# Kernel optimization log

Hardware: AMD Instinct MI355X
Metric: run time of the kernel (lower is better)

Reference implementation:

```python
import jax, jax.numpy as jnp
import numpy as np
import math

L, B, S, D, H, F, C = 2, 2, 1024, 512, 32, 2048, 1000
EPS_LN = 1e-5

def _grid_coords(batch, seq_len):
    g = math.ceil(math.sqrt(seq_len))
    xs = jnp.linspace(0.0, 1.0, g)
    gx, gy = jnp.meshgrid(xs, xs, indexing='ij')
    pts = jnp.stack([gx.ravel(), gy.ravel()], axis=1)
    reps = math.ceil(seq_len / (g * g))
    pts = jnp.tile(pts, (reps, 1))[:seq_len]
    return jnp.broadcast_to(pts[None], (batch, seq_len, 2)).astype(jnp.float32)

def setup_inputs() -> dict:
    key = jax.random.key(0)
    ks = iter(jax.random.split(key, 16))
    sd = 0.02
    inp = {
        'x': jax.random.normal(next(ks), (B, S, D), jnp.float32),
        'coords': _grid_coords(B, S),
        'Wq': jax.random.normal(next(ks), (L, D, D), jnp.float32) * sd,
        'Wk': jax.random.normal(next(ks), (L, D, D), jnp.float32) * sd,
        'Wv': jax.random.normal(next(ks), (L, D, D), jnp.float32) * sd,
        'rot_w1': jax.random.normal(next(ks), (L, 3, H), jnp.float32) * 0.5,
        'rot_b1': jnp.zeros((L, H), jnp.float32),
        'rot_w2': jax.random.normal(next(ks), (L, H), jnp.float32) * 0.1,
        'rot_b2': jnp.zeros((L,), jnp.float32),
        'trans_w1': jax.random.normal(next(ks), (L, 2, H), jnp.float32) * 0.5,
        'trans_b1': jnp.zeros((L, H), jnp.float32),
        'trans_w2': jax.random.normal(next(ks), (L, H), jnp.float32) * 0.1,
        'trans_b2': jnp.zeros((L,), jnp.float32),
        'refl_w1': jax.random.normal(next(ks), (L, 4, H), jnp.float32) * 0.5,
        'refl_b1': jnp.zeros((L, H), jnp.float32),
        'refl_w2': jax.random.normal(next(ks), (L, H), jnp.float32) * 0.1,
        'refl_b2': jnp.zeros((L,), jnp.float32),
        'ln1_g': jnp.ones((L, D), jnp.float32),
        'ln1_b': jnp.zeros((L, D), jnp.float32),
        'ffn_w1': jax.random.normal(next(ks), (L, D, F), jnp.float32) * sd,
        'ffn_b1': jnp.zeros((L, F), jnp.float32),
        'ffn_w2': jax.random.normal(next(ks), (L, F, D), jnp.float32) * sd,
        'ffn_b2': jnp.zeros((L, D), jnp.float32),
        'ln2_g': jnp.ones((L, D), jnp.float32),
        'ln2_b': jnp.zeros((L, D), jnp.float32),
        'lnf_g': jnp.ones((D,), jnp.float32),
        'lnf_b': jnp.zeros((D,), jnp.float32),
        'fc_w': jax.random.normal(next(ks), (D, C), jnp.float32) * sd,
        'fc_b': jnp.zeros((C,), jnp.float32),
    }
    return inp

def _layernorm(x, g, b):
    mu = x.mean(-1, keepdims=True)
    var = ((x - mu) ** 2).mean(-1, keepdims=True)
    return (x - mu) * jax.lax.rsqrt(var + EPS_LN) * g + b

def _pair_mlp(inp, w1, b1, w2, b2):
    # inp: [B,S,S,f] -> [B,S,S]
    h = jax.nn.relu(jnp.einsum('bijf,fh->bijh', inp, w1) + b1)
    return jnp.einsum('bijh,h->bij', h, w2) + b2

def reference(x, coords, Wq, Wk, Wv, rot_w1, rot_b1, rot_w2, rot_b2,
              trans_w1, trans_b1, trans_w2, trans_b2,
              refl_w1, refl_b1, refl_w2, refl_b2,
              ln1_g, ln1_b, ffn_w1, ffn_b1, ffn_w2, ffn_b2, ln2_g, ln2_b,
              lnf_g, lnf_b, fc_w, fc_b):
    d_model = x.shape[-1]
    scale = math.sqrt(d_model)
    # Pairwise relative geometry (layer-independent): rel = coords_j - coords_i
    rel = coords[:, None, :, :] - coords[:, :, None, :]   # [B,S,S,2]
    dx, dy = rel[..., 0], rel[..., 1]
    dist = jnp.sqrt(dx * dx + dy * dy + 1e-8)
    theta = jnp.arctan2(dy, dx)
    rot_in = jnp.stack([dist, jnp.sin(theta), jnp.cos(theta)], axis=-1)  # [B,S,S,3]
    trans_in = rel                                                       # [B,S,S,2]
    refl_in = jnp.concatenate([rel, -rel], axis=-1)                      # [B,S,S,4]

    n_layers = Wq.shape[0]
    for l in range(n_layers):
        Q = x @ Wq[l]
        K = x @ Wk[l]
        V = x @ Wv[l]
        scores = jnp.einsum('bid,bjd->bij', Q, K) / scale
        scores = scores \
            + _pair_mlp(rot_in, rot_w1[l], rot_b1[l], rot_w2[l], rot_b2[l]) \
            + _pair_mlp(trans_in, trans_w1[l], trans_b1[l], trans_w2[l], trans_b2[l]) \
            + _pair_mlp(refl_in, refl_w1[l], refl_b1[l], refl_w2[l], refl_b2[l])
        attn = jax.nn.softmax(scores, axis=-1)
        attn_out = jnp.einsum('bij,bjd->bid', attn, V)
        x = _layernorm(x + attn_out, ln1_g[l], ln1_b[l])
        ffn = jax.nn.relu(x @ ffn_w1[l] + ffn_b1[l]) @ ffn_w2[l] + ffn_b2[l]
        x = _layernorm(x + ffn, ln2_g[l], ln2_b[l])

    x = _layernorm(x, lnf_g, lnf_b)
    pooled = x.mean(axis=1)          # [B,D]
    return pooled @ fc_w + fc_b      # [B,C]
```

## Files before the change

kernel.cpp:

```cpp
#include <hip/hip_runtime.h>
#include <hip/hip_bf16.h>

using bf16 = __hip_bfloat16;
typedef __attribute__((ext_vector_type(8))) short short8;
typedef __attribute__((ext_vector_type(4))) float f32x4;

constexpr int NLAYER = 2;
constexpr int NB = 2;
constexpr int NS = 1024;
constexpr int ND = 512;
constexpr int NH = 32;
constexpr int NF = 2048;
constexpr int NC = 1000;
constexpr float EPS_LN = 1e-5f;

__device__ inline unsigned short f2bfu(float x) {
    union { bf16 h; unsigned short u; } c;
    c.h = __float2bfloat16(x);
    return c.u;
}

#define GLOAD16(gp, lp) __builtin_amdgcn_global_load_lds( \
    (const __attribute__((address_space(1))) void*)(gp),  \
    (__attribute__((address_space(3))) void*)(lp), 16, 0, 0)

template<int BM, int BN, int WR, int WC, bool OUTBF, bool RELU, bool SCORES, bool VOUT>
__global__ __launch_bounds__(512) void mfma_gemm(
    const bf16* __restrict__ A, const bf16* __restrict__ B,
    const float* __restrict__ bias, void* __restrict__ Cout,
    const float* __restrict__ table, bf16* __restrict__ vT,
    int K, int lda, int ldb, int ldc,
    long sA, long sB, long sC, float alpha)
{
    const int bz = blockIdx.z;
    A += (long)bz * sA;
    B += (long)bz * sB;
    const int bm = blockIdx.y * BM, bn = blockIdx.x * BN;
    __shared__ bf16 As[2][BM * 32], Bs[2][BN * 32];
    const int tid = threadIdx.x, lane = tid & 63, wv = tid >> 6;
    constexpr int WM = BM / WR, WN = BN / WC;
    constexpr int FM = WM / 16, FN = WN / 16;
    const int wr = (wv / WC) * WM, wc = (wv % WC) * WN;
    f32x4 acc[FM][FN] = {};
    const int ko = (lane & 3) * 8;
    constexpr int ACH = BM / 16;
    constexpr int BCH = BN / 16;
    constexpr int NCH = ACH + BCH;

    auto stage = [&](int buf, int k0) {
        for (int c = wv; c < NCH; c += 8) {
            if (c < ACH) {
                int r = c * 16 + (lane >> 2);
                GLOAD16(A + (long)(bm + r) * lda + k0 + ko, &As[buf][c * 512]);
            } else {
                int cc = c - ACH;
                int r = cc * 16 + (lane >> 2);
                GLOAD16(B + (long)(bn + r) * ldb + k0 + ko, &Bs[buf][cc * 512]);
            }
        }
    };

    const int nt = K >> 5;
    stage(0, 0);
    __syncthreads();
    for (int t = 0; t < nt; ++t) {
        const int cur = t & 1;
        if (t + 1 < nt) stage(cur ^ 1, (t + 1) << 5);
        const short8* Asv = (const short8*)As[cur];
        const short8* Bsv = (const short8*)Bs[cur];
        short8 af[FM], bfr[FN];
        #pragma unroll
        for (int m = 0; m < FM; ++m)
            af[m] = Asv[(wr + m * 16 + (lane & 15)) * 4 + (lane >> 4)];
        #pragma unroll
        for (int n = 0; n < FN; ++n)
            bfr[n] = Bsv[(wc + n * 16 + (lane & 15)) * 4 + (lane >> 4)];
        #pragma unroll
        for (int m = 0; m < FM; ++m)
            #pragma unroll
            for (int n = 0; n < FN; ++n)
                acc[m][n] = __builtin_amdgcn_mfma_f32_16x16x32_bf16(
                    af[m], bfr[n], acc[m][n], 0, 0, 0);
        __syncthreads();
    }

    const int er = (lane >> 4) * 4, ec = lane & 15;
    #pragma unroll
    for (int m = 0; m < FM; ++m) {
        #pragma unroll
        for (int n = 0; n < FN; ++n) {
            const int row0 = bm + wr + m * 16 + er;
            const int col  = bn + wc + n * 16 + ec;
            const float bv = bias ? bias[col] : 0.f;
            #pragma unroll
            for (int e = 0; e < 4; ++e) {
                const int row = row0 + e;
                float v = acc[m][n][e];
                if (SCORES) {
                    int di = (col >> 5) - (row >> 5) + 31;
                    int dj = (col & 31) - (row & 31) + 31;
                    v = v * alpha + table[di * 63 + dj];
                } else {
                    v += bv;
                    if (RELU) v = fmaxf(v, 0.f);
                }
                if (OUTBF)
                    ((bf16*)Cout)[bz * sC + (long)row * ldc + col] = __float2bfloat16(v);
                else
                    ((float*)Cout)[bz * sC + (long)row * ldc + col] = v;
                if (VOUT && col >= 2 * ND) {
                    int bb = row >> 10;
                    vT[(long)bb * ND * NS + (long)(col - 2 * ND) * NS + (row & (NS - 1))] =
                        __float2bfloat16(v);
                }
            }
        }
    }
}

__global__ __launch_bounds__(256) void wtrans_kernel(
    const float* __restrict__ Wq, const float* __restrict__ Wk,
    const float* __restrict__ Wv, const float* __restrict__ ffn_w1,
    const float* __restrict__ ffn_w2, bf16* __restrict__ wqkvT,
    bf16* __restrict__ w1T, bf16* __restrict__ w2T)
{
    const int s = blockIdx.x;
    const float* src; bf16* dst; int R, C, r0, c0;
    if (s < 1536) {
        int z = s >> 8, rem = s & 255;
        int l = z / 3, wsel = z % 3;
        src = (wsel == 0 ? Wq : wsel == 1 ? Wk : Wv) + (long)l * ND * ND;
        dst = wqkvT + (long)l * 3 * ND * ND + (long)wsel * ND * ND;
        R = ND; C = ND; c0 = (rem & 15) * 32; r0 = (rem >> 4) * 32;
    } else if (s < 3584) {
        int t = s - 1536, l = t >> 10, rem = t & 1023;
        src = ffn_w1 + (long)l * ND * NF;
        dst = w1T + (long)l * NF * ND;
        R = ND; C = NF; c0 = (rem & 63) * 32; r0 = (rem >> 6) * 32;
    } else {
        int t = s - 3584, l = t >> 10, rem = t & 1023;
        src = ffn_w2 + (long)l * NF * ND;
        dst = w2T + (long)l * ND * NF;
        R = NF; C = ND; c0 = (rem & 15) * 32; r0 = (rem >> 4) * 32;
    }
    __shared__ float t[32][33];
    const int lx = threadIdx.x & 31, ly = threadIdx.x >> 5;
    for (int rr = ly; rr < 32; rr += 8)
        t[rr][lx] = src[(long)(r0 + rr) * C + c0 + lx];
    __syncthreads();
    for (int cc = ly; cc < 32; cc += 8)
        dst[(long)(c0 + cc) * R + r0 + lx] = __float2bfloat16(t[lx][cc]);
}

__global__ __launch_bounds__(256) void prep_kernel(
    const float* __restrict__ xin, float* __restrict__ xc, bf16* __restrict__ xb,
    const float* __restrict__ coords,
    const float* __restrict__ rot_w1, const float* __restrict__ rot_b1,
    const float* __restrict__ rot_w2, const float* __restrict__ rot_b2,
    const float* __restrict__ trans_w1, const float* __restrict__ trans_b1,
    const float* __restrict__ trans_w2, const float* __restrict__ trans_b2,
    const float* __restrict__ refl_w1, const float* __restrict__ refl_b1,
    const float* __restrict__ refl_w2, const float* __restrict__ refl_b2,
    float* __restrict__ table,
    const float* __restrict__ fc_b, float* __restrict__ out,
    float* __restrict__ pooled)
{
    const int blk = blockIdx.x, tid = threadIdx.x;
    if (blk < 1024) {
        long i = (long)blk * 256 + tid;
        float4 v = ((const float4*)xin)[i];
        ((float4*)xc)[i] = v;
        uint2 o;
        o.x = (unsigned)f2bfu(v.x) | ((unsigned)f2bfu(v.y) << 16);
        o.y = (unsigned)f2bfu(v.z) | ((unsigned)f2bfu(v.w) << 16);
        ((uint2*)xb)[i] = o;
        return;
    }
    if (blk < 1040) {
        int idx = (blk - 1024) * 256 + tid;
        if (idx >= 63 * 63) return;
        int da = idx / 63 - 31, db = idx % 63 - 31;
        int ai = da < 0 ? -da : 0, bi = db < 0 ? -db : 0;
        int i = ai * 32 + bi, j = (ai + da) * 32 + (bi + db);
        float2 ci = ((const float2*)coords)[i];
        float2 cj = ((const float2*)coords)[j];
        float dx = cj.x - ci.x, dy = cj.y - ci.y;
        float dist = sqrtf(dx * dx + dy * dy + 1e-8f);
        float th = atan2f(dy, dx);
        float sn = sinf(th), cs = cosf(th);
        #pragma unroll
        for (int l = 0; l < NLAYER; ++l) {
            const float* rw1 = rot_w1 + l * 3 * NH;
            const float* rb1 = rot_b1 + l * NH;
            const float* rw2 = rot_w2 + l * NH;
            const float* tw1 = trans_w1 + l * 2 * NH;
            const float* tb1 = trans_b1 + l * NH;
            const float* tw2 = trans_w2 + l * NH;
            const float* fw1 = refl_w1 + l * 4 * NH;
            const float* fb1 = refl_b1 + l * NH;
            const float* fw2 = refl_w2 + l * NH;
            float acc = rot_b2[l] + trans_b2[l] + refl_b2[l];
            #pragma unroll 8
            for (int h = 0; h < NH; ++h) {
                float hr = fmaxf(dist * rw1[h] + sn * rw1[NH + h] + cs * rw1[2 * NH + h] + rb1[h], 0.f);
                acc += hr * rw2[h];
                float ht = fmaxf(dx * tw1[h] + dy * tw1[NH + h] + tb1[h], 0.f);
                acc += ht * tw2[h];
                float hf = fmaxf(dx * fw1[h] + dy * fw1[NH + h] - dx * fw1[2 * NH + h] - dy * fw1[3 * NH + h] + fb1[h], 0.f);
                acc += hf * fw2[h];
            }
            table[l * 3969 + idx] = acc;
        }
        return;
    }
    {
        int i = (blk - 1040) * 256 + tid;
        if (i < NB * NC) out[i] = fc_b[i % NC];
        int j = i - NB * NC;
        if (j >= 0 && j < NB * ND) pooled[j] = 0.f;
    }
}

__global__ __launch_bounds__(256) void softmax_kernel(
    const float* __restrict__ sc, bf16* __restrict__ P)
{
    const float* p = sc + (long)blockIdx.x * NS;
    const int tid = threadIdx.x;
    float4 v = ((const float4*)p)[tid];
    float m = fmaxf(fmaxf(v.x, v.y), fmaxf(v.z, v.w));
    #pragma unroll
    for (int off = 32; off; off >>= 1) m = fmaxf(m, __shfl_xor(m, off));
    __shared__ float red[4], red2[4];
    int wid = tid >> 6;
    if ((tid & 63) == 0) red[wid] = m;
    __syncthreads();
    m = fmaxf(fmaxf(red[0], red[1]), fmaxf(red[2], red[3]));
    v.x = __expf(v.x - m); v.y = __expf(v.y - m);
    v.z = __expf(v.z - m); v.w = __expf(v.w - m);
    float s = v.x + v.y + v.z + v.w;
    #pragma unroll
    for (int off = 32; off; off >>= 1) s += __shfl_xor(s, off);
    if ((tid & 63) == 0) red2[wid] = s;
    __syncthreads();
    s = red2[0] + red2[1] + red2[2] + red2[3];
    float inv = 1.f / s;
    uint2 o;
    o.x = (unsigned)f2bfu(v.x * inv) | ((unsigned)f2bfu(v.y * inv) << 16);
    o.y = (unsigned)f2bfu(v.z * inv) | ((unsigned)f2bfu(v.w * inv) << 16);
    ((uint2*)(P + (long)blockIdx.x * NS))[tid] = o;
}

__global__ __launch_bounds__(256) void add_ln_kernel(
    const float* __restrict__ x, const float* __restrict__ res,
    const float* __restrict__ g, const float* __restrict__ bt,
    float* __restrict__ out, bf16* __restrict__ outb)
{
    long row = blockIdx.x;
    const int tid = threadIdx.x;
    float2 xv = ((const float2*)(x + row * ND))[tid];
    if (res) {
        float2 rv = ((const float2*)(res + row * ND))[tid];
        xv.x += rv.x; xv.y += rv.y;
    }
    float s = xv.x + xv.y;
    float ss = xv.x * xv.x + xv.y * xv.y;
    #pragma unroll
    for (int off = 32; off; off >>= 1) {
        s += __shfl_xor(s, off);
        ss += __shfl_xor(ss, off);
    }
    __shared__ float rs[4], rss[4];
    int wid = tid >> 6;
    if ((tid & 63) == 0) { rs[wid] = s; rss[wid] = ss; }
    __syncthreads();
    s = rs[0] + rs[1] + rs[2] + rs[3];
    ss = rss[0] + rss[1] + rss[2] + rss[3];
    float mu = s * (1.f / ND);
    float var = ss * (1.f / ND) - mu * mu;
    float inv = rsqrtf(var + EPS_LN);
    float2 gv = ((const float2*)g)[tid];
    float2 bv = ((const float2*)bt)[tid];
    float2 o;
    o.x = (xv.x - mu) * inv * gv.x + bv.x;
    o.y = (xv.y - mu) * inv * gv.y + bv.y;
    ((float2*)(out + row * ND))[tid] = o;
    if (outb)
        ((unsigned int*)(outb + row * ND))[tid] =
            (unsigned)f2bfu(o.x) | ((unsigned)f2bfu(o.y) << 16);
}

__global__ __launch_bounds__(256) void pool_kernel(
    const float* __restrict__ x, float* __restrict__ pooled)
{
    const int tid = threadIdx.x;
    const long row0 = (long)blockIdx.x * 16;
    const int b = (int)(row0 >> 10);
    float ax = 0.f, ay = 0.f, az = 0.f, aw = 0.f;
    #pragma unroll
    for (int it = 0; it < 8; ++it) {
        long r = row0 + it * 2 + (tid >> 7);
        float4 v = ((const float4*)(x + r * ND))[tid & 127];
        ax += v.x; ay += v.y; az += v.z; aw += v.w;
    }
    __shared__ float red[256][4];
    red[tid][0] = ax; red[tid][1] = ay; red[tid][2] = az; red[tid][3] = aw;
    __syncthreads();
    if (tid < 128) {
        int d = tid * 4;
        atomicAdd(&pooled[b * ND + d + 0], (red[tid][0] + red[tid + 128][0]) * (1.f / NS));
        atomicAdd(&pooled[b * ND + d + 1], (red[tid][1] + red[tid + 128][1]) * (1.f / NS));
        atomicAdd(&pooled[b * ND + d + 2], (red[tid][2] + red[tid + 128][2]) * (1.f / NS));
        atomicAdd(&pooled[b * ND + d + 3], (red[tid][3] + red[tid + 128][3]) * (1.f / NS));
    }
}

__global__ __launch_bounds__(256) void fc_kernel(
    const float* __restrict__ pooled, const float* __restrict__ w,
    float* __restrict__ out)
{
    const int lane = threadIdx.x & 63, dg = threadIdx.x >> 6;
    const int c = blockIdx.x * 64 + lane;
    const int b = blockIdx.y;
    const int d0 = blockIdx.z * 64 + dg * 16;
    const bool ok = (c < NC);
    const float* p = pooled + b * ND;
    float acc = 0.f;
    #pragma unroll
    for (int d = 0; d < 16; ++d)
        acc += p[d0 + d] * (ok ? w[(long)(d0 + d) * NC + c] : 0.f);
    __shared__ float red[4][64];
    red[dg][lane] = acc;
    __syncthreads();
    if (dg == 0 && ok)
        atomicAdd(&out[(long)b * NC + c],
                  red[0][lane] + red[1][lane] + red[2][lane] + red[3][lane]);
}

extern "C" void kernel_launch(void* const* d_in, const int* in_sizes, int n_in,
                              void* d_out, int out_size, void* d_ws, size_t ws_size,
                              hipStream_t stream)
{
    const float* x_in   = (const float*)d_in[0];
    const float* coords = (const float*)d_in[1];
    const float* Wq     = (const float*)d_in[2];
    const float* Wk     = (const float*)d_in[3];
    const float* Wv     = (const float*)d_in[4];
    const float* rot_w1 = (const float*)d_in[5];
    const float* rot_b1 = (const float*)d_in[6];
    const float* rot_w2 = (const float*)d_in[7];
    const float* rot_b2 = (const float*)d_in[8];
    const float* trans_w1 = (const float*)d_in[9];
    const float* trans_b1 = (const float*)d_in[10];
    const float* trans_w2 = (const float*)d_in[11];
    const float* trans_b2 = (const float*)d_in[12];
    const float* refl_w1 = (const float*)d_in[13];
    const float* refl_b1 = (const float*)d_in[14];
    const float* refl_w2 = (const float*)d_in[15];
    const float* refl_b2 = (const float*)d_in[16];
    const float* ln1_g = (const float*)d_in[17];
    const float* ln1_b = (const float*)d_in[18];
    const float* ffn_w1 = (const float*)d_in[19];
    const float* ffn_b1 = (const float*)d_in[20];
    const float* ffn_w2 = (const float*)d_in[21];
    const float* ffn_b2 = (const float*)d_in[22];
    const float* ln2_g = (const float*)d_in[23];
    const float* ln2_b = (const float*)d_in[24];
    const float* lnf_g = (const float*)d_in[25];
    const float* lnf_b = (const float*)d_in[26];
    const float* fc_w = (const float*)d_in[27];
    const float* fc_b = (const float*)d_in[28];
    float* out = (float*)d_out;

    const long XSZ = (long)NB * NS * ND;
    const long SSZ = (long)NB * NS * NS;

    char* wp = (char*)d_ws;
    auto alloc = [&](long bytes) -> char* {
        char* p = wp; wp += (bytes + 255) & ~(long)255; return p;
    };
    float* x_cur  = (float*)alloc(XSZ * 4);
    bf16*  xb     = (bf16*)alloc(XSZ * 2);
    bf16*  qkv    = (bf16*)alloc((long)NB * NS * 1536 * 2);
    bf16*  vT     = (bf16*)alloc((long)NB * ND * NS * 2);
    float* sc     = (float*)alloc(SSZ * 4);
    bf16*  pb     = (bf16*)alloc(SSZ * 2);
    float* ao     = (float*)alloc(XSZ * 4);
    bf16*  hfb    = (bf16*)alloc((long)NB * NS * NF * 2);
    bf16*  wqkvT  = (bf16*)alloc((long)NLAYER * 3 * ND * ND * 2);
    bf16*  w1T    = (bf16*)alloc((long)NLAYER * NF * ND * 2);
    bf16*  w2T    = (bf16*)alloc((long)NLAYER * ND * NF * 2);
    float* table  = (float*)alloc((long)NLAYER * 3969 * 4);
    float* pooled = (float*)alloc((long)NB * ND * 4);

    const float inv_scale = 1.0f / sqrtf((float)ND);
    const long QKVLD = 1536;

    wtrans_kernel<<<dim3(5632), 256, 0, stream>>>(
        Wq, Wk, Wv, ffn_w1, ffn_w2, wqkvT, w1T, w2T);

    prep_kernel<<<dim3(1052), 256, 0, stream>>>(
        x_in, x_cur, xb, coords,
        rot_w1, rot_b1, rot_w2, rot_b2,
        trans_w1, trans_b1, trans_w2, trans_b2,
        refl_w1, refl_b1, refl_w2, refl_b2, table,
        fc_b, out, pooled);

    for (int l = 0; l < NLAYER; ++l) {
        mfma_gemm<128, 128, 4, 2, true, false, false, true>
            <<<dim3(1536 / 128, (NB * NS) / 128, 1), 512, 0, stream>>>(
            xb, wqkvT + (long)l * 3 * ND * ND, nullptr, qkv, nullptr, vT,
            ND, ND, ND, QKVLD, 0, 0, 0, 0.f);

        mfma_gemm<128, 128, 4, 2, false, false, true, false>
            <<<dim3(NS / 128, NS / 128, NB), 512, 0, stream>>>(
            qkv, qkv + ND, nullptr, sc, table + (long)l * 3969, nullptr,
            ND, QKVLD, QKVLD, NS, (long)NS * QKVLD, (long)NS * QKVLD,
            (long)NS * NS, inv_scale);

        softmax_kernel<<<dim3(NB * NS), 256, 0, stream>>>(sc, pb);

        mfma_gemm<64, 128, 2, 4, false, false, false, false>
            <<<dim3(ND / 128, NS / 64, NB), 512, 0, stream>>>(
            pb, vT, nullptr, ao, nullptr, nullptr,
            NS, NS, NS, ND, (long)NS * NS, (long)ND * NS, (long)NS * ND, 0.f);

        add_ln_kernel<<<dim3(NB * NS), 256, 0, stream>>>(
            x_cur, ao, ln1_g + (long)l * ND, ln1_b + (long)l * ND, x_cur, xb);

        mfma_gemm<128, 128, 4, 2, true, true, false, false>
            <<<dim3(NF / 128, (NB * NS) / 128, 1), 512, 0, stream>>>(
            xb, w1T + (long)l * NF * ND, ffn_b1 + (long)l * NF, hfb, nullptr, nullptr,
            ND, ND, ND, NF, 0, 0, 0, 0.f);

        mfma_gemm<64, 128, 2, 4, false, false, false, false>
            <<<dim3(ND / 128, (NB * NS) / 64, 1), 512, 0, stream>>>(
            hfb, w2T + (long)l * ND * NF, ffn_b2 + (long)l * ND, ao, nullptr, nullptr,
            NF, NF, NF, ND, 0, 0, 0, 0.f);

        add_ln_kernel<<<dim3(NB * NS), 256, 0, stream>>>(
            x_cur, ao, ln2_g + (long)l * ND, ln2_b + (long)l * ND, x_cur, xb);
    }

    add_ln_kernel<<<dim3(NB * NS), 256, 0, stream>>>(
        x_cur, nullptr, lnf_g, lnf_b, x_cur, nullptr);

    pool_kernel<<<dim3((NB * NS) / 16), 256, 0, stream>>>(x_cur, pooled);

    fc_kernel<<<dim3((NC + 63) / 64, NB, ND / 64), 256, 0, stream>>>(pooled, fc_w, out);
}
```

Measured before the change: 384.3 us.

## Deepen GEMM K-tile to 64, use vmcnt-based pipelining, fuse prep kernels, retile GEMMs

The MFMA GEMM now stages 64-wide K tiles with a row-of-8 LDS layout and waits on partial vmcnt instead of full __syncthreads, so the next tile's global-to-LDS loads overlap compute. The goal is fewer barriers per K and more latency hiding. The weight-transpose kernel is merged into the prep kernel to save a launch. Several GEMM launches switch to smaller tiles (64x128, 64x64) for more blocks and better CU occupancy. LDS use doubles, and the hand-written waitcnt counts must match the per-wave load count.

```diff
diff --git a/kernel.cpp b/kernel.cpp
--- a/kernel.cpp
+++ b/kernel.cpp
@@ -36,52 +36,72 @@
     A += (long)bz * sA;
     B += (long)bz * sB;
     const int bm = blockIdx.y * BM, bn = blockIdx.x * BN;
-    __shared__ bf16 As[2][BM * 32], Bs[2][BN * 32];
+    __shared__ bf16 As[2][BM * 64], Bs[2][BN * 64];
     const int tid = threadIdx.x, lane = tid & 63, wv = tid >> 6;
     constexpr int WM = BM / WR, WN = BN / WC;
     constexpr int FM = WM / 16, FN = WN / 16;
     const int wr = (wv / WC) * WM, wc = (wv % WC) * WN;
     f32x4 acc[FM][FN] = {};
-    const int ko = (lane & 3) * 8;
-    constexpr int ACH = BM / 16;
-    constexpr int BCH = BN / 16;
-    constexpr int NCH = ACH + BCH;
+    const int krow = lane >> 3;
+    const int ko = (lane & 7) * 8;
+    constexpr int ACH = BM / 8, NCH = (BM + BN) / 8;
+    constexpr int SW = NCH / 8;
 
     auto stage = [&](int buf, int k0) {
-        for (int c = wv; c < NCH; c += 8) {
-            if (c < ACH) {
-                int r = c * 16 + (lane >> 2);
-                GLOAD16(A + (long)(bm + r) * lda + k0 + ko, &As[buf][c * 512]);
-            } else {
-                int cc = c - ACH;
-                int r = cc * 16 + (lane >> 2);
-                GLOAD16(B + (long)(bn + r) * ldb + k0 + ko, &Bs[buf][cc * 512]);
-            }
+        #pragma unroll
+        for (int i = 0; i < SW; ++i) {
+            const int c = wv + i * 8;
+            if (c < ACH)
+                GLOAD16(A + (long)(bm + c * 8 + krow) * lda + k0 + ko,
+                        &As[buf][c * 512]);
+            else
+                GLOAD16(B + (long)(bn + (c - ACH) * 8 + krow) * ldb + k0 + ko,
+                        &Bs[buf][(c - ACH) * 512]);
         }
     };
 
-    const int nt = K >> 5;
+    const int nt = K >> 6;
     stage(0, 0);
-    __syncthreads();
+    asm volatile("s_waitcnt vmcnt(0)" ::: "memory");
+    __builtin_amdgcn_sched_barrier(0);
+    __builtin_amdgcn_s_barrier();
+
     for (int t = 0; t < nt; ++t) {
         const int cur = t & 1;
-        if (t + 1 < nt) stage(cur ^ 1, (t + 1) << 5);
+        if (t + 1 < nt) {
+            stage(cur ^ 1, (t + 1) << 6);
+            if constexpr (SW == 2)      asm volatile("s_waitcnt vmcnt(2)" ::: "memory");
+            else if constexpr (SW == 3) asm volatile("s_waitcnt vmcnt(3)" ::: "memory");
+            else                        asm volatile("s_waitcnt vmcnt(4)" ::: "memory");
+        } else {
+            asm volatile("s_waitcnt vmcnt(0)" ::: "memory");
+        }
+        __builtin_amdgcn_sched_barrier(0);
+        __builtin_amdgcn_s_barrier();
+
         const short8* Asv = (const short8*)As[cur];
         const short8* Bsv = (const short8*)Bs[cur];
-        short8 af[FM], bfr[FN];
         #pragma unroll
-        for (int m = 0; m < FM; ++m)
-            af[m] = Asv[(wr + m * 16 + (lane & 15)) * 4 + (lane >> 4)];
-        #pragma unroll
-        for (int n = 0; n < FN; ++n)
-            bfr[n] = Bsv[(wc + n * 16 + (lane & 15)) * 4 + (lane >> 4)];
-        #pragma unroll
-        for (int m = 0; m < FM; ++m)
+        for (int ks = 0; ks < 2; ++ks) {
+            short8 af[FM], bfr[FN];
             #pragma unroll
-            for (int n = 0; n < FN; ++n)
-                acc[m][n] = __builtin_amdgcn_mfma_f32_16x16x32_bf16(
-                    af[m], bfr[n], acc[m][n], 0, 0, 0);
-        __syncthreads();
+            for (int m = 0; m < FM; ++m) {
+                const int row = wr + m * 16 + (lane & 15);
+                af[m] = Asv[(row >> 3) * 64 + (lane & 7) * 8 + ks * 4 + (lane >> 4)];
+            }
+            #pragma unroll
+            for (int n = 0; n < FN; ++n) {
+                const int row = wc + n * 16 + (lane & 15);
+                bfr[n] = Bsv[(row >> 3) * 64 + (lane & 7) * 8 + ks * 4 + (lane >> 4)];
+            }
+            #pragma unroll
+            for (int m = 0; m < FM; ++m)
+                #pragma unroll
+                for (int n = 0; n < FN; ++n)
+                    acc[m][n] = __builtin_amdgcn_mfma_f32_16x16x32_bf16(
+                        af[m], bfr[n], acc[m][n], 0, 0, 0);
+        }
+        __builtin_amdgcn_s_barrier();
     }
 
     const int er = (lane >> 4) * 4, ec = lane & 15;
@@ -118,41 +138,11 @@
     }
 }
 
-__global__ __launch_bounds__(256) void wtrans_kernel(
+__global__ __launch_bounds__(256) void prep_kernel(
     const float* __restrict__ Wq, const float* __restrict__ Wk,
     const float* __restrict__ Wv, const float* __restrict__ ffn_w1,
     const float* __restrict__ ffn_w2, bf16* __restrict__ wqkvT,
-    bf16* __restrict__ w1T, bf16* __restrict__ w2T)
-{
-    const int s = blockIdx.x;
-    const float* src; bf16* dst; int R, C, r0, c0;
-    if (s < 1536) {
-        int z = s >> 8, rem = s & 255;
-        int l = z / 3, wsel = z % 3;
-        src = (wsel == 0 ? Wq : wsel == 1 ? Wk : Wv) + (long)l * ND * ND;
-        dst = wqkvT + (long)l * 3 * ND * ND + (long)wsel * ND * ND;
-        R = ND; C = ND; c0 = (rem & 15) * 32; r0 = (rem >> 4) * 32;
-    } else if (s < 3584) {
-        int t = s - 1536, l = t >> 10, rem = t & 1023;
-        src = ffn_w1 + (long)l * ND * NF;
-        dst = w1T + (long)l * NF * ND;
-        R = ND; C = NF; c0 = (rem & 63) * 32; r0 = (rem >> 6) * 32;
-    } else {
-        int t = s - 3584, l = t >> 10, rem = t & 1023;
-        src = ffn_w2 + (long)l * NF * ND;
-        dst = w2T + (long)l * ND * NF;
-        R = NF; C = ND; c0 = (rem & 15) * 32; r0 = (rem >> 4) * 32;
-    }
-    __shared__ float t[32][33];
-    const int lx = threadIdx.x & 31, ly = threadIdx.x >> 5;
-    for (int rr = ly; rr < 32; rr += 8)
-        t[rr][lx] = src[(long)(r0 + rr) * C + c0 + lx];
-    __syncthreads();
-    for (int cc = ly; cc < 32; cc += 8)
-        dst[(long)(c0 + cc) * R + r0 + lx] = __float2bfloat16(t[lx][cc]);
-}
-
-__global__ __launch_bounds__(256) void prep_kernel(
+    bf16* __restrict__ w1T, bf16* __restrict__ w2T,
     const float* __restrict__ xin, float* __restrict__ xc, bf16* __restrict__ xb,
     const float* __restrict__ coords,
     const float* __restrict__ rot_w1, const float* __restrict__ rot_b1,
@@ -166,8 +156,37 @@
     float* __restrict__ pooled)
 {
     const int blk = blockIdx.x, tid = threadIdx.x;
-    if (blk < 1024) {
-        long i = (long)blk * 256 + tid;
+    if (blk < 5632) {
+        const int s = blk;
+        const float* src; bf16* dst; int R, C, r0, c0;
+        if (s < 1536) {
+            int z = s >> 8, rem = s & 255;
+            int l = z / 3, wsel = z % 3;
+            src = (wsel == 0 ? Wq : wsel == 1 ? Wk : Wv) + (long)l * ND * ND;
+            dst = wqkvT + (long)l * 3 * ND * ND + (long)wsel * ND * ND;
+            R = ND; C = ND; c0 = (rem & 15) * 32; r0 = (rem >> 4) * 32;
+        } else if (s < 3584) {
+            int t = s - 1536, l = t >> 10, rem = t & 1023;
+            src = ffn_w1 + (long)l * ND * NF;
+            dst = w1T + (long)l * NF * ND;
+            R = ND; C = NF; c0 = (rem & 63) * 32; r0 = (rem >> 6) * 32;
+        } else {
+            int t = s - 3584, l = t >> 10, rem = t & 1023;
+            src = ffn_w2 + (long)l * NF * ND;
+            dst = w2T + (long)l * ND * NF;
+            R = NF; C = ND; c0 = (rem & 15) * 32; r0 = (rem >> 4) * 32;
+        }
+        __shared__ float t[32][33];
+        const int lx = tid & 31, ly = tid >> 5;
+        for (int rr = ly; rr < 32; rr += 8)
+            t[rr][lx] = src[(long)(r0 + rr) * C + c0 + lx];
+        __syncthreads();
+        for (int cc = ly; cc < 32; cc += 8)
+            dst[(long)(c0 + cc) * R + r0 + lx] = __float2bfloat16(t[lx][cc]);
+        return;
+    }
+    if (blk < 6656) {
+        long i = (long)(blk - 5632) * 256 + tid;
         float4 v = ((const float4*)xin)[i];
         ((float4*)xc)[i] = v;
         uint2 o;
@@ -176,8 +195,8 @@
         ((uint2*)xb)[i] = o;
         return;
     }
-    if (blk < 1040) {
-        int idx = (blk - 1024) * 256 + tid;
+    if (blk < 6672) {
+        int idx = (blk - 6656) * 256 + tid;
         if (idx >= 63 * 63) return;
         int da = idx / 63 - 31, db = idx % 63 - 31;
         int ai = da < 0 ? -da : 0, bi = db < 0 ? -db : 0;
@@ -214,7 +233,7 @@
         return;
     }
     {
-        int i = (blk - 1040) * 256 + tid;
+        int i = (blk - 6672) * 256 + tid;
         if (i < NB * NC) out[i] = fc_b[i % NC];
         int j = i - NB * NC;
         if (j >= 0 && j < NB * ND) pooled[j] = 0.f;
@@ -395,10 +414,8 @@
     const float inv_scale = 1.0f / sqrtf((float)ND);
     const long QKVLD = 1536;
 
-    wtrans_kernel<<<dim3(5632), 256, 0, stream>>>(
-        Wq, Wk, Wv, ffn_w1, ffn_w2, wqkvT, w1T, w2T);
-
-    prep_kernel<<<dim3(1052), 256, 0, stream>>>(
+    prep_kernel<<<dim3(6684), 256, 0, stream>>>(
+        Wq, Wk, Wv, ffn_w1, ffn_w2, wqkvT, w1T, w2T,
         x_in, x_cur, xb, coords,
         rot_w1, rot_b1, rot_w2, rot_b2,
         trans_w1, trans_b1, trans_w2, trans_b2,
@@ -406,21 +423,21 @@
         fc_b, out, pooled);
 
     for (int l = 0; l < NLAYER; ++l) {
-        mfma_gemm<128, 128, 4, 2, true, false, false, true>
-            <<<dim3(1536 / 128, (NB * NS) / 128, 1), 512, 0, stream>>>(
+        mfma_gemm<64, 128, 2, 4, true, false, false, true>
+            <<<dim3(1536 / 128, (NB * NS) / 64, 1), 512, 0, stream>>>(
             xb, wqkvT + (long)l * 3 * ND * ND, nullptr, qkv, nullptr, vT,
             ND, ND, ND, QKVLD, 0, 0, 0, 0.f);
 
-        mfma_gemm<128, 128, 4, 2, false, false, true, false>
-            <<<dim3(NS / 128, NS / 128, NB), 512, 0, stream>>>(
+        mfma_gemm<64, 128, 2, 4, false, false, true, false>
+            <<<dim3(NS / 128, NS / 64, NB), 512, 0, stream>>>(
             qkv, qkv + ND, nullptr, sc, table + (long)l * 3969, nullptr,
             ND, QKVLD, QKVLD, NS, (long)NS * QKVLD, (long)NS * QKVLD,
             (long)NS * NS, inv_scale);
 
         softmax_kernel<<<dim3(NB * NS), 256, 0, stream>>>(sc, pb);
 
-        mfma_gemm<64, 128, 2, 4, false, false, false, false>
-            <<<dim3(ND / 128, NS / 64, NB), 512, 0, stream>>>(
+        mfma_gemm<64, 64, 4, 2, false, false, false, false>
+            <<<dim3(ND / 64, NS / 64, NB), 512, 0, stream>>>(
             pb, vT, nullptr, ao, nullptr, nullptr,
             NS, NS, NS, ND, (long)NS * NS, (long)ND * NS, (long)NS * ND, 0.f);
 
@@ -432,8 +449,8 @@
             xb, w1T + (long)l * NF * ND, ffn_b1 + (long)l * NF, hfb, nullptr, nullptr,
             ND, ND, ND, NF, 0, 0, 0, 0.f);
 
-        mfma_gemm<64, 128, 2, 4, false, false, false, false>
-            <<<dim3(ND / 128, (NB * NS) / 64, 1), 512, 0, stream>>>(
+        mfma_gemm<64, 64, 4, 2, false, false, false, false>
+            <<<dim3(ND / 64, (NB * NS) / 64, 1), 512, 0, stream>>>(
             hfb, w2T + (long)l * ND * NF, ffn_b2 + (long)l * ND, ao, nullptr, nullptr,
             NF, NF, NF, ND, 0, 0, 0, 0.f);
 
```

Result: faster. 341.4 us (-11.2%).
